# Optimization experiments

Hardware: AMD Instinct MI355X
Metric: run time of the kernel (lower is better)

## Reference

```python
import jax, jax.numpy as jnp
import numpy as np

MEMORY_SIZE = 8192
FEATURE_DIM = 512
NUM_QUERIES = 32768
EPS = 1e-12  # guard for sqrt in cdist


def setup_inputs() -> dict:
    key = jax.random.key(0)
    k1, k2, k3, k4 = jax.random.split(key, 4)
    return {
        "features": jax.random.normal(k1, (MEMORY_SIZE, FEATURE_DIM), dtype=jnp.float32),
        "positions": jax.random.normal(k2, (MEMORY_SIZE, 3), dtype=jnp.float32),
        "query_positions": jax.random.normal(k3, (NUM_QUERIES, 3), dtype=jnp.float32),
        "position_embeddings": jax.random.normal(k4, (MEMORY_SIZE, 3), dtype=jnp.float32),
    }


def _cdist(a, b):
    # Euclidean distance via ||a||^2 + ||b||^2 - 2 a.b; avoids [Q,M,3] intermediate.
    a2 = jnp.sum(a * a, axis=-1, keepdims=True)          # [Q,1]
    b2 = jnp.sum(b * b, axis=-1, keepdims=True).T        # [1,M]
    d2 = a2 + b2 - 2.0 * (a @ b.T)                       # [Q,M]
    return jnp.sqrt(jnp.maximum(d2, EPS))


def reference(features, positions, query_positions, position_embeddings):
    # --- update ---
    positions_norm = positions / jnp.linalg.norm(positions, axis=-1, keepdims=True)
    embeddings_norm = position_embeddings / jnp.linalg.norm(position_embeddings, axis=-1, keepdims=True)
    sim = positions_norm @ embeddings_norm.T             # [M,M]
    attn = jax.nn.softmax(sim, axis=-1)
    memory = attn @ features                              # [M,F]
    new_pos_emb = attn @ positions                        # [M,3]
    # --- query ---
    dist = _cdist(query_positions, new_pos_emb)           # [Q,M]
    qattn = jax.nn.softmax(-dist, axis=-1)
    retrieved = qattn @ memory                            # [Q,F]
    return retrieved
```

## Files before the change

kernel.cpp:

```cpp
#include <hip/hip_runtime.h>
#include <stdint.h>
#include <stddef.h>

#define M_SZ 8192
#define F_DIM 512
#define N_Q 32768

typedef __attribute__((ext_vector_type(4))) float f32x4;
typedef __attribute__((ext_vector_type(8))) __bf16 bf16x8;
typedef __attribute__((ext_vector_type(2))) __bf16 bf16x2;

__device__ __forceinline__ float bits_to_f(unsigned u) {
    union { unsigned u; float f; } v; v.u = u; return v.f;
}
__device__ __forceinline__ unsigned pk_bf16(float a, float b) {
    union { bf16x2 v; unsigned u; } cv;
    cv.v.x = (__bf16)a; cv.v.y = (__bf16)b;
    return cv.u;
}
__device__ __forceinline__ unsigned short f2bf(float x) {
    union { bf16x2 v; unsigned u; } cv;
    cv.v.x = (__bf16)x; cv.v.y = (__bf16)0.0f;
    return (unsigned short)(cv.u & 0xffffu);
}
__device__ __forceinline__ bf16x8 as_bf16x8(uint4 u) {
    union { uint4 a; bf16x8 b; } cv; cv.a = u; return cv.b;
}

__global__ void prep_kernel(const float* __restrict__ pos,
                            const float* __restrict__ emb,
                            float* __restrict__ pn4,
                            float* __restrict__ en4,
                            float* __restrict__ pos4) {
    int i = blockIdx.x * 256 + threadIdx.x;
    if (i >= M_SZ) return;
    float x = pos[i * 3 + 0], y = pos[i * 3 + 1], z = pos[i * 3 + 2];
    float inv = 1.0f / __builtin_amdgcn_sqrtf(x * x + y * y + z * z);
    pn4[i * 4 + 0] = x * inv; pn4[i * 4 + 1] = y * inv;
    pn4[i * 4 + 2] = z * inv; pn4[i * 4 + 3] = 0.0f;
    pos4[i * 4 + 0] = x; pos4[i * 4 + 1] = y;
    pos4[i * 4 + 2] = z; pos4[i * 4 + 3] = 0.0f;
    float ex = emb[i * 3 + 0], ey = emb[i * 3 + 1], ez = emb[i * 3 + 2];
    float einv = 1.0f / __builtin_amdgcn_sqrtf(ex * ex + ey * ey + ez * ez);
    en4[i * 4 + 0] = ex * einv; en4[i * 4 + 1] = ey * einv;
    en4[i * 4 + 2] = ez * einv; en4[i * 4 + 3] = 0.0f;
}

__global__ void transpose_kernel(const float* __restrict__ feat,
                                 unsigned short* __restrict__ featT) {
    __shared__ float tile[64 * 65];
    const int jb = blockIdx.x * 64, fb = blockIdx.y * 64;
    const int t = threadIdx.x;
#pragma unroll
    for (int p = 0; p < 16; ++p) {
        int idx = p * 256 + t;
        int j = idx >> 6, f = idx & 63;
        tile[j * 65 + f] = feat[(size_t)(jb + j) * F_DIM + fb + f];
    }
    __syncthreads();
#pragma unroll
    for (int p = 0; p < 16; ++p) {
        int idx = p * 256 + t;
        int f = idx >> 6, j = idx & 63;
        featT[(size_t)(fb + f) * M_SZ + jb + j] = f2bf(tile[j * 65 + f]);
    }
}

__launch_bounds__(512, 2)
__global__ void build_memory_kernel(const float* __restrict__ pn4,
                                    const float* __restrict__ en4,
                                    const float* __restrict__ pos4,
                                    const unsigned short* __restrict__ featT,
                                    unsigned short* __restrict__ memT,
                                    float* __restrict__ npe4) {
    constexpr int BM = 32, BK = 32, PSTR = BK + 8;
    __shared__ unsigned short pbuf[2][BM * PSTR];
    __shared__ f32x4 red4[512];
    __shared__ float lbuf[BM];

    const int t = threadIdx.x;
    const int lane = t & 63, wv = t >> 6;
    const int col = lane & 15, quad = lane >> 4;
    const int mb = blockIdx.x * BM;
    const int r = t & 31, jq = t >> 5;

    const f32x4 pnr = ((const f32x4*)pn4)[mb + r];
    const f32x4* en = (const f32x4*)en4;
    const f32x4* ps = (const f32x4*)pos4;

    const unsigned short* bp[4];
#pragma unroll
    for (int n = 0; n < 4; ++n)
        bp[n] = featT + (size_t)(wv * 64 + n * 16 + col) * M_SZ + quad * 8;

    f32x4 acc[2][4];
    const f32x4 zero4 = {0.f, 0.f, 0.f, 0.f};
#pragma unroll
    for (int m = 0; m < 2; ++m)
#pragma unroll
        for (int n = 0; n < 4; ++n) acc[m][n] = zero4;
    float nx = 0.f, ny = 0.f, nz = 0.f, lp = 0.f;

    uint4 vbA[4], vbB[4];
#pragma unroll
    for (int n = 0; n < 4; ++n) vbA[n] = *(const uint4*)(bp[n]);

#define B_GEN_P(JB, SIDE)                                                    \
    {                                                                        \
        int j = (JB) + jq * 2;                                               \
        f32x4 e0 = en[j], e1 = en[j + 1];                                    \
        f32x4 p0 = ps[j], p1 = ps[j + 1];                                    \
        float s0 = fmaf(pnr.x, e0.x, fmaf(pnr.y, e0.y, pnr.z * e0.z));       \
        float s1 = fmaf(pnr.x, e1.x, fmaf(pnr.y, e1.y, pnr.z * e1.z));       \
        float w0 = __builtin_amdgcn_exp2f(s0 * 1.44269504f);                 \
        float w1 = __builtin_amdgcn_exp2f(s1 * 1.44269504f);                 \
        unsigned u = pk_bf16(w0, w1);                                        \
        float w0r = bits_to_f(u << 16), w1r = bits_to_f(u & 0xffff0000u);    \
        lp += w0r + w1r;                                                     \
        nx = fmaf(w0r, p0.x, fmaf(w1r, p1.x, nx));                           \
        ny = fmaf(w0r, p0.y, fmaf(w1r, p1.y, ny));                           \
        nz = fmaf(w0r, p0.z, fmaf(w1r, p1.z, nz));                           \
        *(unsigned*)(&pbuf[SIDE][r * PSTR + jq * 2]) = u;                    \
    }

#define B_MFMA(VB, SIDE)                                                     \
    {                                                                        \
        _Pragma("unroll") for (int m = 0; m < 2; ++m) {                      \
            bf16x8 a = *(const bf16x8*)(&pbuf[SIDE][(m * 16 + col) * PSTR + quad * 8]); \
            _Pragma("unroll") for (int n = 0; n < 4; ++n)                    \
                acc[m][n] = __builtin_amdgcn_mfma_f32_16x16x32_bf16(         \
                    a, as_bf16x8(VB[n]), acc[m][n], 0, 0, 0);                \
        }                                                                    \
    }

#define B_BODY(CUR, NXT, SIDE, JNXT)                                         \
    {                                                                        \
        _Pragma("unroll") for (int n = 0; n < 4; ++n) {                      \
            NXT[n] = *(const uint4*)(bp[n] + BK);                            \
            bp[n] += BK;                                                     \
        }                                                                    \
        B_GEN_P(JNXT, SIDE ^ 1)                                              \
        B_MFMA(CUR, SIDE)                                                    \
        __syncthreads();                                                     \
    }

    B_GEN_P(0, 0)
    __syncthreads();

    int jn = BK;
    for (int kt = 0; kt < 254; kt += 2) {
        B_BODY(vbA, vbB, 0, jn) jn += BK;
        B_BODY(vbB, vbA, 1, jn) jn += BK;
    }
    B_BODY(vbA, vbB, 0, jn)
    B_MFMA(vbB, 1)
#undef B_BODY
#undef B_MFMA
#undef B_GEN_P

    f32x4 mine = {nx, ny, nz, lp};
    red4[t] = mine;
    __syncthreads();
    if (t < BM) {
        f32x4 s = red4[t];
#pragma unroll
        for (int g = 1; g < 16; ++g) {
            f32x4 o = red4[t + 32 * g];
            s.x += o.x; s.y += o.y; s.z += o.z; s.w += o.w;
        }
        lbuf[t] = s.w;
        float inv = 1.0f / s.w;
        float X = s.x * inv, Y = s.y * inv, Z = s.z * inv;
        f32x4 o = {X, Y, Z, X * X + Y * Y + Z * Z};
        ((f32x4*)npe4)[mb + t] = o;
    }
    __syncthreads();

#pragma unroll
    for (int m = 0; m < 2; ++m) {
        f32x4 l4 = *(const f32x4*)(lbuf + m * 16 + quad * 4);
        f32x4 inv4 = {1.0f / l4.x, 1.0f / l4.y, 1.0f / l4.z, 1.0f / l4.w};
        int mg = mb + m * 16 + quad * 4;
#pragma unroll
        for (int n = 0; n < 4; ++n) {
            int fg = wv * 64 + n * 16 + col;
            uint2 o;
            o.x = pk_bf16(acc[m][n].x * inv4.x, acc[m][n].y * inv4.y);
            o.y = pk_bf16(acc[m][n].z * inv4.z, acc[m][n].w * inv4.w);
            *(uint2*)(memT + (size_t)fg * M_SZ + mg) = o;
        }
    }
}

__launch_bounds__(512, 2)
__global__ void query_kernel(const float* __restrict__ qpos,
                             const float* __restrict__ npe4,
                             const unsigned short* __restrict__ memT,
                             float* __restrict__ out) {
    constexpr int BM = 128, BK = 32, PSTR = BK + 8;
    __shared__ unsigned short pbuf[2][BM * PSTR];
    __shared__ float redl[512];
    __shared__ float lbuf[BM];

    const int t = threadIdx.x;
    const int lane = t & 63, wv = t >> 6;
    const int col = lane & 15, quad = lane >> 4;
    const int qb = blockIdx.x * BM;
    const int r = t & 127, jq = t >> 7;

    const float qx = qpos[(size_t)(qb + r) * 3 + 0];
    const float qy = qpos[(size_t)(qb + r) * 3 + 1];
    const float qz = qpos[(size_t)(qb + r) * 3 + 2];
    const float q2 = qx * qx + qy * qy + qz * qz;
    const float m2x = -2.0f * qx, m2y = -2.0f * qy, m2z = -2.0f * qz;

    const f32x4* nsrc = (const f32x4*)npe4;

    const unsigned short* bp[4];
#pragma unroll
    for (int n = 0; n < 4; ++n)
        bp[n] = memT + (size_t)(wv * 64 + n * 16 + col) * M_SZ + quad * 8;

    f32x4 acc[8][4];
    const f32x4 zero4 = {0.f, 0.f, 0.f, 0.f};
#pragma unroll
    for (int m = 0; m < 8; ++m)
#pragma unroll
        for (int n = 0; n < 4; ++n) acc[m][n] = zero4;
    float lp = 0.f;

    uint4 vbA[4], vbB[4];
#pragma unroll
    for (int n = 0; n < 4; ++n) vbA[n] = *(const uint4*)(bp[n]);

#define Q_GEN_P(JB, SIDE)                                                    \
    {                                                                        \
        unsigned pk4[4];                                                     \
        _Pragma("unroll") for (int i = 0; i < 8; i += 2) {                   \
            int j = (JB) + jq * 8 + i;                                       \
            f32x4 n0 = nsrc[j], n1 = nsrc[j + 1];                            \
            float s0 = fmaf(m2x, n0.x, fmaf(m2y, n0.y, fmaf(m2z, n0.z, q2 + n0.w))); \
            float s1 = fmaf(m2x, n1.x, fmaf(m2y, n1.y, fmaf(m2z, n1.z, q2 + n1.w))); \
            s0 = fmaxf(s0, 1e-12f); s1 = fmaxf(s1, 1e-12f);                  \
            float w0 = __builtin_amdgcn_exp2f(__builtin_amdgcn_sqrtf(s0) * -1.44269504f); \
            float w1 = __builtin_amdgcn_exp2f(__builtin_amdgcn_sqrtf(s1) * -1.44269504f); \
            unsigned u = pk_bf16(w0, w1);                                    \
            lp += bits_to_f(u << 16) + bits_to_f(u & 0xffff0000u);           \
            pk4[i >> 1] = u;                                                 \
        }                                                                    \
        *(uint4*)(&pbuf[SIDE][r * PSTR + jq * 8]) =                          \
            make_uint4(pk4[0], pk4[1], pk4[2], pk4[3]);                      \
    }

#define Q_MFMA(VB, SIDE)                                                     \
    {                                                                        \
        _Pragma("unroll") for (int m = 0; m < 8; ++m) {                      \
            bf16x8 a = *(const bf16x8*)(&pbuf[SIDE][(m * 16 + col) * PSTR + quad * 8]); \
            _Pragma("unroll") for (int n = 0; n < 4; ++n)                    \
                acc[m][n] = __builtin_amdgcn_mfma_f32_16x16x32_bf16(         \
                    a, as_bf16x8(VB[n]), acc[m][n], 0, 0, 0);                \
        }                                                                    \
    }

#define Q_BODY(CUR, NXT, SIDE, JNXT)                                         \
    {                                                                        \
        _Pragma("unroll") for (int n = 0; n < 4; ++n) {                      \
            NXT[n] = *(const uint4*)(bp[n] + BK);                            \
            bp[n] += BK;                                                     \
        }                                                                    \
        Q_GEN_P(JNXT, SIDE ^ 1)                                              \
        Q_MFMA(CUR, SIDE)                                                    \
        __syncthreads();                                                     \
    }

    Q_GEN_P(0, 0)
    __syncthreads();

    int jn = BK;
    for (int kt = 0; kt < 254; kt += 2) {
        Q_BODY(vbA, vbB, 0, jn) jn += BK;
        Q_BODY(vbB, vbA, 1, jn) jn += BK;
    }
    Q_BODY(vbA, vbB, 0, jn)
    Q_MFMA(vbB, 1)
#undef Q_BODY
#undef Q_MFMA
#undef Q_GEN_P

    redl[t] = lp;
    __syncthreads();
    if (t < BM) lbuf[t] = redl[t] + redl[t + 128] + redl[t + 256] + redl[t + 384];
    __syncthreads();

#pragma unroll
    for (int m = 0; m < 8; ++m) {
        f32x4 l4 = *(const f32x4*)(lbuf + m * 16 + quad * 4);
        f32x4 inv4 = {1.0f / l4.x, 1.0f / l4.y, 1.0f / l4.z, 1.0f / l4.w};
        int qg = qb + m * 16 + quad * 4;
#pragma unroll
        for (int n = 0; n < 4; ++n) {
            int fg = wv * 64 + n * 16 + col;
            out[(size_t)(qg + 0) * F_DIM + fg] = acc[m][n].x * inv4.x;
            out[(size_t)(qg + 1) * F_DIM + fg] = acc[m][n].y * inv4.y;
            out[(size_t)(qg + 2) * F_DIM + fg] = acc[m][n].z * inv4.z;
            out[(size_t)(qg + 3) * F_DIM + fg] = acc[m][n].w * inv4.w;
        }
    }
}

extern "C" void kernel_launch(void* const* d_in, const int* in_sizes, int n_in,
                              void* d_out, int out_size, void* d_ws, size_t ws_size,
                              hipStream_t stream) {
    const float* features  = (const float*)d_in[0];
    const float* positions = (const float*)d_in[1];
    const float* qpos      = (const float*)d_in[2];
    const float* pemb      = (const float*)d_in[3];
    float* out = (float*)d_out;
    char* ws = (char*)d_ws;

    unsigned short* featT = (unsigned short*)(ws);
    unsigned short* memT  = (unsigned short*)(ws + 8388608);
    float* npe4 = (float*)(ws + 16777216);
    float* pn4  = (float*)(ws + 16908288);
    float* en4  = (float*)(ws + 17039360);
    float* pos4 = (float*)(ws + 17170432);

    hipLaunchKernelGGL(prep_kernel, dim3(M_SZ / 256), dim3(256), 0, stream,
                       positions, pemb, pn4, en4, pos4);
    hipLaunchKernelGGL(transpose_kernel, dim3(M_SZ / 64, F_DIM / 64), dim3(256), 0, stream,
                       features, featT);
    hipLaunchKernelGGL(build_memory_kernel, dim3(M_SZ / 32), dim3(512), 0, stream,
                       pn4, en4, pos4, featT, memT, npe4);
    hipLaunchKernelGGL(query_kernel, dim3(N_Q / 128), dim3(512), 0, stream,
                       qpos, npe4, memT, out);
}
```

Measured before the change: 816.3 us.

## Retile build and query kernels to 256-thread blocks with setprio MFMA sections

The build kernel now runs with 256 threads and is split over a second grid dimension covering halves of the feature axis. Only the first half computes the new position embeddings, so the softmax weights are recomputed in both halves. The query kernel shrinks its query tile from 128 to 64 rows and widens each wave's feature tile to 128 columns. Both kernels drop the register double-buffering of B fragments in favour of a single buffer, and wrap their MFMA sections in s_setprio. The aim is more blocks and better occupancy, at the cost of less A-tile reuse, duplicated exp work in the build kernel, and more exposed global load latency.

Result: slower. 1.056 ms (+29.4%).

```diff
diff --git a/kernel.cpp b/kernel.cpp
--- a/kernel.cpp
+++ b/kernel.cpp
@@ -66,7 +66,7 @@
     }
 }
 
-__launch_bounds__(512, 2)
+__launch_bounds__(256, 2)
 __global__ void build_memory_kernel(const float* __restrict__ pn4,
                                     const float* __restrict__ en4,
                                     const float* __restrict__ pos4,
@@ -75,13 +75,14 @@
                                     float* __restrict__ npe4) {
     constexpr int BM = 32, BK = 32, PSTR = BK + 8;
     __shared__ unsigned short pbuf[2][BM * PSTR];
-    __shared__ f32x4 red4[512];
+    __shared__ f32x4 red4[256];
     __shared__ float lbuf[BM];
 
     const int t = threadIdx.x;
     const int lane = t & 63, wv = t >> 6;
     const int col = lane & 15, quad = lane >> 4;
     const int mb = blockIdx.x * BM;
+    const int yh = blockIdx.y;
     const int r = t & 31, jq = t >> 5;
 
     const f32x4 pnr = ((const f32x4*)pn4)[mb + r];
@@ -91,7 +92,7 @@
     const unsigned short* bp[4];
 #pragma unroll
     for (int n = 0; n < 4; ++n)
-        bp[n] = featT + (size_t)(wv * 64 + n * 16 + col) * M_SZ + quad * 8;
+        bp[n] = featT + (size_t)(yh * 256 + wv * 64 + n * 16 + col) * M_SZ + quad * 8;
 
     f32x4 acc[2][4];
     const f32x4 zero4 = {0.f, 0.f, 0.f, 0.f};
@@ -101,62 +102,79 @@
         for (int n = 0; n < 4; ++n) acc[m][n] = zero4;
     float nx = 0.f, ny = 0.f, nz = 0.f, lp = 0.f;
 
-    uint4 vbA[4], vbB[4];
-#pragma unroll
-    for (int n = 0; n < 4; ++n) vbA[n] = *(const uint4*)(bp[n]);
-
-#define B_GEN_P(JB, SIDE)                                                    \
-    {                                                                        \
-        int j = (JB) + jq * 2;                                               \
-        f32x4 e0 = en[j], e1 = en[j + 1];                                    \
-        f32x4 p0 = ps[j], p1 = ps[j + 1];                                    \
-        float s0 = fmaf(pnr.x, e0.x, fmaf(pnr.y, e0.y, pnr.z * e0.z));       \
-        float s1 = fmaf(pnr.x, e1.x, fmaf(pnr.y, e1.y, pnr.z * e1.z));       \
-        float w0 = __builtin_amdgcn_exp2f(s0 * 1.44269504f);                 \
-        float w1 = __builtin_amdgcn_exp2f(s1 * 1.44269504f);                 \
-        unsigned u = pk_bf16(w0, w1);                                        \
-        float w0r = bits_to_f(u << 16), w1r = bits_to_f(u & 0xffff0000u);    \
-        lp += w0r + w1r;                                                     \
-        nx = fmaf(w0r, p0.x, fmaf(w1r, p1.x, nx));                           \
-        ny = fmaf(w0r, p0.y, fmaf(w1r, p1.y, ny));                           \
-        nz = fmaf(w0r, p0.z, fmaf(w1r, p1.z, nz));                           \
-        *(unsigned*)(&pbuf[SIDE][r * PSTR + jq * 2]) = u;                    \
-    }
-
-#define B_MFMA(VB, SIDE)                                                     \
-    {                                                                        \
+    uint4 vb[4];
+
+#define B_COMP(SIDE)                                                         \
+    {                                                                        \
+        float w_[4];                                                         \
+        _Pragma("unroll") for (int i = 0; i < 4; ++i) {                      \
+            float s = fmaf(pnr.x, ee[i].x, fmaf(pnr.y, ee[i].y, pnr.z * ee[i].z)); \
+            w_[i] = __builtin_amdgcn_exp2f(s * 1.44269504f);                 \
+        }                                                                    \
+        unsigned u0 = pk_bf16(w_[0], w_[1]), u1 = pk_bf16(w_[2], w_[3]);     \
+        float wr0 = bits_to_f(u0 << 16), wr1 = bits_to_f(u0 & 0xffff0000u);  \
+        float wr2 = bits_to_f(u1 << 16), wr3 = bits_to_f(u1 & 0xffff0000u);  \
+        lp += (wr0 + wr1) + (wr2 + wr3);                                     \
+        if (yh == 0) {                                                       \
+            nx = fmaf(wr0, pp[0].x, fmaf(wr1, pp[1].x, fmaf(wr2, pp[2].x, fmaf(wr3, pp[3].x, nx)))); \
+            ny = fmaf(wr0, pp[0].y, fmaf(wr1, pp[1].y, fmaf(wr2, pp[2].y, fmaf(wr3, pp[3].y, ny)))); \
+            nz = fmaf(wr0, pp[0].z, fmaf(wr1, pp[1].z, fmaf(wr2, pp[2].z, fmaf(wr3, pp[3].z, nz)))); \
+        }                                                                    \
+        *(uint2*)(&pbuf[SIDE][r * PSTR + jq * 4]) = make_uint2(u0, u1);      \
+    }
+
+#define B_MFMA(SIDE)                                                         \
+    {                                                                        \
+        __builtin_amdgcn_s_setprio(1);                                       \
         _Pragma("unroll") for (int m = 0; m < 2; ++m) {                      \
             bf16x8 a = *(const bf16x8*)(&pbuf[SIDE][(m * 16 + col) * PSTR + quad * 8]); \
             _Pragma("unroll") for (int n = 0; n < 4; ++n)                    \
                 acc[m][n] = __builtin_amdgcn_mfma_f32_16x16x32_bf16(         \
-                    a, as_bf16x8(VB[n]), acc[m][n], 0, 0, 0);                \
-        }                                                                    \
-    }
-
-#define B_BODY(CUR, NXT, SIDE, JNXT)                                         \
-    {                                                                        \
+                    a, as_bf16x8(vb[n]), acc[m][n], 0, 0, 0);                \
+        }                                                                    \
+        __builtin_amdgcn_s_setprio(0);                                       \
+    }
+
+#define B_BODY(SIDE, JNXT)                                                   \
+    {                                                                        \
+        f32x4 ee[4], pp[4];                                                  \
+        _Pragma("unroll") for (int i = 0; i < 4; ++i) {                      \
+            ee[i] = en[(JNXT) + jq * 4 + i];                                 \
+            pp[i] = ps[(JNXT) + jq * 4 + i];                                 \
+        }                                                                    \
         _Pragma("unroll") for (int n = 0; n < 4; ++n) {                      \
-            NXT[n] = *(const uint4*)(bp[n] + BK);                            \
-            bp[n] += BK;                                                     \
-        }                                                                    \
-        B_GEN_P(JNXT, SIDE ^ 1)                                              \
-        B_MFMA(CUR, SIDE)                                                    \
+            vb[n] = *(const uint4*)(bp[n]);  bp[n] += BK;                    \
+        }                                                                    \
+        B_COMP(SIDE ^ 1)                                                     \
+        B_MFMA(SIDE)                                                         \
         __syncthreads();                                                     \
     }
 
-    B_GEN_P(0, 0)
+    {
+        f32x4 ee[4], pp[4];
+#pragma unroll
+        for (int i = 0; i < 4; ++i) {
+            ee[i] = en[jq * 4 + i];
+            pp[i] = ps[jq * 4 + i];
+        }
+        B_COMP(0)
+    }
     __syncthreads();
 
     int jn = BK;
     for (int kt = 0; kt < 254; kt += 2) {
-        B_BODY(vbA, vbB, 0, jn) jn += BK;
-        B_BODY(vbB, vbA, 1, jn) jn += BK;
-    }
-    B_BODY(vbA, vbB, 0, jn)
-    B_MFMA(vbB, 1)
+        B_BODY(0, jn) jn += BK;
+        B_BODY(1, jn) jn += BK;
+    }
+    B_BODY(0, jn)
+    {
+#pragma unroll
+        for (int n = 0; n < 4; ++n) vb[n] = *(const uint4*)(bp[n]);
+        B_MFMA(1)
+    }
 #undef B_BODY
 #undef B_MFMA
-#undef B_GEN_P
+#undef B_COMP
 
     f32x4 mine = {nx, ny, nz, lp};
     red4[t] = mine;
@@ -164,15 +182,17 @@
     if (t < BM) {
         f32x4 s = red4[t];
 #pragma unroll
-        for (int g = 1; g < 16; ++g) {
+        for (int g = 1; g < 8; ++g) {
             f32x4 o = red4[t + 32 * g];
             s.x += o.x; s.y += o.y; s.z += o.z; s.w += o.w;
         }
         lbuf[t] = s.w;
-        float inv = 1.0f / s.w;
-        float X = s.x * inv, Y = s.y * inv, Z = s.z * inv;
-        f32x4 o = {X, Y, Z, X * X + Y * Y + Z * Z};
-        ((f32x4*)npe4)[mb + t] = o;
+        if (yh == 0) {
+            float inv = 1.0f / s.w;
+            float X = s.x * inv, Y = s.y * inv, Z = s.z * inv;
+            f32x4 o = {X, Y, Z, X * X + Y * Y + Z * Z};
+            ((f32x4*)npe4)[mb + t] = o;
+        }
     }
     __syncthreads();
 
@@ -183,7 +203,7 @@
         int mg = mb + m * 16 + quad * 4;
 #pragma unroll
         for (int n = 0; n < 4; ++n) {
-            int fg = wv * 64 + n * 16 + col;
+            int fg = yh * 256 + wv * 64 + n * 16 + col;
             uint2 o;
             o.x = pk_bf16(acc[m][n].x * inv4.x, acc[m][n].y * inv4.y);
             o.y = pk_bf16(acc[m][n].z * inv4.z, acc[m][n].w * inv4.w);
@@ -192,21 +212,21 @@
     }
 }
 
-__launch_bounds__(512, 2)
+__launch_bounds__(256, 2)
 __global__ void query_kernel(const float* __restrict__ qpos,
                              const float* __restrict__ npe4,
                              const unsigned short* __restrict__ memT,
                              float* __restrict__ out) {
-    constexpr int BM = 128, BK = 32, PSTR = BK + 8;
+    constexpr int BM = 64, BK = 32, PSTR = BK + 8;
     __shared__ unsigned short pbuf[2][BM * PSTR];
-    __shared__ float redl[512];
+    __shared__ float redl[256];
     __shared__ float lbuf[BM];
 
     const int t = threadIdx.x;
     const int lane = t & 63, wv = t >> 6;
     const int col = lane & 15, quad = lane >> 4;
     const int qb = blockIdx.x * BM;
-    const int r = t & 127, jq = t >> 7;
+    const int r = t & 63, jq = t >> 6;
 
     const float qx = qpos[(size_t)(qb + r) * 3 + 0];
     const float qy = qpos[(size_t)(qb + r) * 3 + 1];
@@ -216,31 +236,27 @@
 
     const f32x4* nsrc = (const f32x4*)npe4;
 
-    const unsigned short* bp[4];
-#pragma unroll
-    for (int n = 0; n < 4; ++n)
-        bp[n] = memT + (size_t)(wv * 64 + n * 16 + col) * M_SZ + quad * 8;
-
-    f32x4 acc[8][4];
+    const unsigned short* bp[8];
+#pragma unroll
+    for (int n = 0; n < 8; ++n)
+        bp[n] = memT + (size_t)(wv * 128 + n * 16 + col) * M_SZ + quad * 8;
+
+    f32x4 acc[4][8];
     const f32x4 zero4 = {0.f, 0.f, 0.f, 0.f};
 #pragma unroll
-    for (int m = 0; m < 8; ++m)
-#pragma unroll
-        for (int n = 0; n < 4; ++n) acc[m][n] = zero4;
+    for (int m = 0; m < 4; ++m)
+#pragma unroll
+        for (int n = 0; n < 8; ++n) acc[m][n] = zero4;
     float lp = 0.f;
 
-    uint4 vbA[4], vbB[4];
-#pragma unroll
-    for (int n = 0; n < 4; ++n) vbA[n] = *(const uint4*)(bp[n]);
-
-#define Q_GEN_P(JB, SIDE)                                                    \
+    uint4 vb[8];
+
+#define Q_COMP(SIDE)                                                         \
     {                                                                        \
         unsigned pk4[4];                                                     \
         _Pragma("unroll") for (int i = 0; i < 8; i += 2) {                   \
-            int j = (JB) + jq * 8 + i;                                       \
-            f32x4 n0 = nsrc[j], n1 = nsrc[j + 1];                            \
-            float s0 = fmaf(m2x, n0.x, fmaf(m2y, n0.y, fmaf(m2z, n0.z, q2 + n0.w))); \
-            float s1 = fmaf(m2x, n1.x, fmaf(m2y, n1.y, fmaf(m2z, n1.z, q2 + n1.w))); \
+            float s0 = fmaf(m2x, nn[i].x, fmaf(m2y, nn[i].y, fmaf(m2z, nn[i].z, q2 + nn[i].w))); \
+            float s1 = fmaf(m2x, nn[i + 1].x, fmaf(m2y, nn[i + 1].y, fmaf(m2z, nn[i + 1].z, q2 + nn[i + 1].w))); \
             s0 = fmaxf(s0, 1e-12f); s1 = fmaxf(s1, 1e-12f);                  \
             float w0 = __builtin_amdgcn_exp2f(__builtin_amdgcn_sqrtf(s0) * -1.44269504f); \
             float w1 = __builtin_amdgcn_exp2f(__builtin_amdgcn_sqrtf(s1) * -1.44269504f); \
@@ -252,54 +268,67 @@
             make_uint4(pk4[0], pk4[1], pk4[2], pk4[3]);                      \
     }
 
-#define Q_MFMA(VB, SIDE)                                                     \
-    {                                                                        \
-        _Pragma("unroll") for (int m = 0; m < 8; ++m) {                      \
+#define Q_MFMA(SIDE)                                                         \
+    {                                                                        \
+        __builtin_amdgcn_s_setprio(1);                                       \
+        _Pragma("unroll") for (int m = 0; m < 4; ++m) {                      \
             bf16x8 a = *(const bf16x8*)(&pbuf[SIDE][(m * 16 + col) * PSTR + quad * 8]); \
-            _Pragma("unroll") for (int n = 0; n < 4; ++n)                    \
+            _Pragma("unroll") for (int n = 0; n < 8; ++n)                    \
                 acc[m][n] = __builtin_amdgcn_mfma_f32_16x16x32_bf16(         \
-                    a, as_bf16x8(VB[n]), acc[m][n], 0, 0, 0);                \
-        }                                                                    \
-    }
-
-#define Q_BODY(CUR, NXT, SIDE, JNXT)                                         \
-    {                                                                        \
-        _Pragma("unroll") for (int n = 0; n < 4; ++n) {                      \
-            NXT[n] = *(const uint4*)(bp[n] + BK);                            \
-            bp[n] += BK;                                                     \
-        }                                                                    \
-        Q_GEN_P(JNXT, SIDE ^ 1)                                              \
-        Q_MFMA(CUR, SIDE)                                                    \
+                    a, as_bf16x8(vb[n]), acc[m][n], 0, 0, 0);                \
+        }                                                                    \
+        __builtin_amdgcn_s_setprio(0);                                       \
+    }
+
+#define Q_BODY(SIDE, JNXT)                                                   \
+    {                                                                        \
+        f32x4 nn[8];                                                         \
+        _Pragma("unroll") for (int i = 0; i < 8; ++i)                        \
+            nn[i] = nsrc[(JNXT) + jq * 8 + i];                               \
+        _Pragma("unroll") for (int n = 0; n < 8; ++n) {                      \
+            vb[n] = *(const uint4*)(bp[n]);  bp[n] += BK;                    \
+        }                                                                    \
+        Q_COMP(SIDE ^ 1)                                                     \
+        Q_MFMA(SIDE)                                                         \
         __syncthreads();                                                     \
     }
 
-    Q_GEN_P(0, 0)
+    {
+        f32x4 nn[8];
+#pragma unroll
+        for (int i = 0; i < 8; ++i) nn[i] = nsrc[jq * 8 + i];
+        Q_COMP(0)
+    }
     __syncthreads();
 
     int jn = BK;
     for (int kt = 0; kt < 254; kt += 2) {
-        Q_BODY(vbA, vbB, 0, jn) jn += BK;
-        Q_BODY(vbB, vbA, 1, jn) jn += BK;
-    }
-    Q_BODY(vbA, vbB, 0, jn)
-    Q_MFMA(vbB, 1)
+        Q_BODY(0, jn) jn += BK;
+        Q_BODY(1, jn) jn += BK;
+    }
+    Q_BODY(0, jn)
+    {
+#pragma unroll
+        for (int n = 0; n < 8; ++n) vb[n] = *(const uint4*)(bp[n]);
+        Q_MFMA(1)
+    }
 #undef Q_BODY
 #undef Q_MFMA
-#undef Q_GEN_P
+#undef Q_COMP
 
     redl[t] = lp;
     __syncthreads();
-    if (t < BM) lbuf[t] = redl[t] + redl[t + 128] + redl[t + 256] + redl[t + 384];
-    __syncthreads();
-
-#pragma unroll
-    for (int m = 0; m < 8; ++m) {
+    if (t < BM) lbuf[t] = redl[t] + redl[t + 64] + redl[t + 128] + redl[t + 192];
+    __syncthreads();
+
+#pragma unroll
+    for (int m = 0; m < 4; ++m) {
         f32x4 l4 = *(const f32x4*)(lbuf + m * 16 + quad * 4);
         f32x4 inv4 = {1.0f / l4.x, 1.0f / l4.y, 1.0f / l4.z, 1.0f / l4.w};
         int qg = qb + m * 16 + quad * 4;
 #pragma unroll
-        for (int n = 0; n < 4; ++n) {
-            int fg = wv * 64 + n * 16 + col;
+        for (int n = 0; n < 8; ++n) {
+            int fg = wv * 128 + n * 16 + col;
             out[(size_t)(qg + 0) * F_DIM + fg] = acc[m][n].x * inv4.x;
             out[(size_t)(qg + 1) * F_DIM + fg] = acc[m][n].y * inv4.y;
             out[(size_t)(qg + 2) * F_DIM + fg] = acc[m][n].z * inv4.z;
@@ -329,8 +358,8 @@
                        positions, pemb, pn4, en4, pos4);
     hipLaunchKernelGGL(transpose_kernel, dim3(M_SZ / 64, F_DIM / 64), dim3(256), 0, stream,
                        features, featT);
-    hipLaunchKernelGGL(build_memory_kernel, dim3(M_SZ / 32), dim3(512), 0, stream,
+    hipLaunchKernelGGL(build_memory_kernel, dim3(M_SZ / 32, 2), dim3(256), 0, stream,
                        pn4, en4, pos4, featT, memT, npe4);
-    hipLaunchKernelGGL(query_kernel, dim3(N_Q / 128), dim3(512), 0, stream,
+    hipLaunchKernelGGL(query_kernel, dim3(N_Q / 64), dim3(256), 0, stream,
                        qpos, npe4, memT, out);
 }
```

## Retile memory-build GEMM to 128 rows by 128 features and double K-step

Applied to the files above, without the earlier changes.

The build kernel moves from 32-row blocks covering all 512 features to 128-row blocks that each cover a quarter of the feature dimension, with four blocks per row group. Each block now computes four times as many softmax weights per feature-column load and issues eight MFMAs per B fragment instead of two. Both the build and query kernels double the K-step from 32 to 64, which halves the number of barriers and loop iterations. The trade-off is that the exp and softmax weight work in the build kernel is now repeated four times across the feature splits, and more registers are used per wave.

After: 887.4 us. +8.7%, slower.

```diff
diff --git a/kernel.cpp b/kernel.cpp
--- a/kernel.cpp
+++ b/kernel.cpp
@@ -73,7 +73,7 @@
                                     const unsigned short* __restrict__ featT,
                                     unsigned short* __restrict__ memT,
                                     float* __restrict__ npe4) {
-    constexpr int BM = 32, BK = 32, PSTR = BK + 8;
+    constexpr int BM = 128, BK = 64, PSTR = BK + 8;
     __shared__ unsigned short pbuf[2][BM * PSTR];
     __shared__ f32x4 red4[512];
     __shared__ float lbuf[BM];
@@ -81,82 +81,92 @@
     const int t = threadIdx.x;
     const int lane = t & 63, wv = t >> 6;
     const int col = lane & 15, quad = lane >> 4;
-    const int mb = blockIdx.x * BM;
-    const int r = t & 31, jq = t >> 5;
+    const int bid = blockIdx.x;
+    const int fb = bid & 3;
+    const int mb = (bid >> 2) * BM;
+    const int r = t & 127, jq = t >> 7;
 
     const f32x4 pnr = ((const f32x4*)pn4)[mb + r];
     const f32x4* en = (const f32x4*)en4;
     const f32x4* ps = (const f32x4*)pos4;
 
-    const unsigned short* bp[4];
-#pragma unroll
-    for (int n = 0; n < 4; ++n)
-        bp[n] = featT + (size_t)(wv * 64 + n * 16 + col) * M_SZ + quad * 8;
-
-    f32x4 acc[2][4];
+    const unsigned short* bp =
+        featT + (size_t)(fb * 128 + wv * 16 + col) * M_SZ + quad * 8;
+
+    f32x4 acc[8];
     const f32x4 zero4 = {0.f, 0.f, 0.f, 0.f};
 #pragma unroll
-    for (int m = 0; m < 2; ++m)
-#pragma unroll
-        for (int n = 0; n < 4; ++n) acc[m][n] = zero4;
+    for (int m = 0; m < 8; ++m) acc[m] = zero4;
     float nx = 0.f, ny = 0.f, nz = 0.f, lp = 0.f;
 
-    uint4 vbA[4], vbB[4];
-#pragma unroll
-    for (int n = 0; n < 4; ++n) vbA[n] = *(const uint4*)(bp[n]);
-
-#define B_GEN_P(JB, SIDE)                                                    \
-    {                                                                        \
-        int j = (JB) + jq * 2;                                               \
-        f32x4 e0 = en[j], e1 = en[j + 1];                                    \
-        f32x4 p0 = ps[j], p1 = ps[j + 1];                                    \
-        float s0 = fmaf(pnr.x, e0.x, fmaf(pnr.y, e0.y, pnr.z * e0.z));       \
-        float s1 = fmaf(pnr.x, e1.x, fmaf(pnr.y, e1.y, pnr.z * e1.z));       \
-        float w0 = __builtin_amdgcn_exp2f(s0 * 1.44269504f);                 \
-        float w1 = __builtin_amdgcn_exp2f(s1 * 1.44269504f);                 \
-        unsigned u = pk_bf16(w0, w1);                                        \
-        float w0r = bits_to_f(u << 16), w1r = bits_to_f(u & 0xffff0000u);    \
-        lp += w0r + w1r;                                                     \
-        nx = fmaf(w0r, p0.x, fmaf(w1r, p1.x, nx));                           \
-        ny = fmaf(w0r, p0.y, fmaf(w1r, p1.y, ny));                           \
-        nz = fmaf(w0r, p0.z, fmaf(w1r, p1.z, nz));                           \
-        *(unsigned*)(&pbuf[SIDE][r * PSTR + jq * 2]) = u;                    \
-    }
-
-#define B_MFMA(VB, SIDE)                                                     \
-    {                                                                        \
-        _Pragma("unroll") for (int m = 0; m < 2; ++m) {                      \
-            bf16x8 a = *(const bf16x8*)(&pbuf[SIDE][(m * 16 + col) * PSTR + quad * 8]); \
-            _Pragma("unroll") for (int n = 0; n < 4; ++n)                    \
-                acc[m][n] = __builtin_amdgcn_mfma_f32_16x16x32_bf16(         \
-                    a, as_bf16x8(VB[n]), acc[m][n], 0, 0, 0);                \
-        }                                                                    \
-    }
-
-#define B_BODY(CUR, NXT, SIDE, JNXT)                                         \
-    {                                                                        \
-        _Pragma("unroll") for (int n = 0; n < 4; ++n) {                      \
-            NXT[n] = *(const uint4*)(bp[n] + BK);                            \
-            bp[n] += BK;                                                     \
-        }                                                                    \
-        B_GEN_P(JNXT, SIDE ^ 1)                                              \
-        B_MFMA(CUR, SIDE)                                                    \
+    uint4 h0A, h0B, h1v;
+    h0A = *(const uint4*)(bp);
+
+#define B_COMP(JB, SIDE)                                                     \
+    {                                                                        \
+        _Pragma("unroll") for (int hh = 0; hh < 2; ++hh) {                   \
+            unsigned us[4];                                                  \
+            _Pragma("unroll") for (int i = 0; i < 8; i += 2) {               \
+                int j = (JB) + jq * 16 + hh * 8 + i;                         \
+                f32x4 e0 = en[j], e1 = en[j + 1];                            \
+                f32x4 p0 = ps[j], p1 = ps[j + 1];                            \
+                float s0 = fmaf(pnr.x, e0.x, fmaf(pnr.y, e0.y, pnr.z * e0.z)); \
+                float s1 = fmaf(pnr.x, e1.x, fmaf(pnr.y, e1.y, pnr.z * e1.z)); \
+                float w0 = __builtin_amdgcn_exp2f(s0 * 1.44269504f);         \
+                float w1 = __builtin_amdgcn_exp2f(s1 * 1.44269504f);         \
+                unsigned u = pk_bf16(w0, w1);                                \
+                float w0r = bits_to_f(u << 16), w1r = bits_to_f(u & 0xffff0000u); \
+                lp += w0r + w1r;                                             \
+                nx = fmaf(w0r, p0.x, fmaf(w1r, p1.x, nx));                   \
+                ny = fmaf(w0r, p0.y, fmaf(w1r, p1.y, ny));                   \
+                nz = fmaf(w0r, p0.z, fmaf(w1r, p1.z, nz));                   \
+                us[i >> 1] = u;                                              \
+            }                                                                \
+            *(uint4*)(&pbuf[(SIDE)][r * PSTR + jq * 16 + hh * 8]) =          \
+                make_uint4(us[0], us[1], us[2], us[3]);                      \
+        }                                                                    \
+    }
+
+#define B_MFMA(SIDE, VB0, VB1)                                               \
+    {                                                                        \
+        _Pragma("unroll") for (int m = 0; m < 8; ++m) {                      \
+            bf16x8 a = *(const bf16x8*)(&pbuf[(SIDE)][(m * 16 + col) * PSTR + quad * 8]); \
+            acc[m] = __builtin_amdgcn_mfma_f32_16x16x32_bf16(                \
+                a, as_bf16x8(VB0), acc[m], 0, 0, 0);                         \
+        }                                                                    \
+        _Pragma("unroll") for (int m = 0; m < 8; ++m) {                      \
+            bf16x8 a = *(const bf16x8*)(&pbuf[(SIDE)][(m * 16 + col) * PSTR + 32 + quad * 8]); \
+            acc[m] = __builtin_amdgcn_mfma_f32_16x16x32_bf16(                \
+                a, as_bf16x8(VB1), acc[m], 0, 0, 0);                         \
+        }                                                                    \
+    }
+
+#define B_BODY(CURH0, NXTH0, SIDE, JNXT)                                     \
+    {                                                                        \
+        h1v = *(const uint4*)(bp + 32);                                      \
+        NXTH0 = *(const uint4*)(bp + 64);                                    \
+        bp += 64;                                                            \
+        B_COMP(JNXT, (SIDE) ^ 1)                                             \
+        B_MFMA(SIDE, CURH0, h1v)                                             \
         __syncthreads();                                                     \
     }
 
-    B_GEN_P(0, 0)
+    B_COMP(0, 0)
     __syncthreads();
 
     int jn = BK;
-    for (int kt = 0; kt < 254; kt += 2) {
-        B_BODY(vbA, vbB, 0, jn) jn += BK;
-        B_BODY(vbB, vbA, 1, jn) jn += BK;
-    }
-    B_BODY(vbA, vbB, 0, jn)
-    B_MFMA(vbB, 1)
+    for (int kt = 0; kt < 126; kt += 2) {
+        B_BODY(h0A, h0B, 0, jn) jn += BK;
+        B_BODY(h0B, h0A, 1, jn) jn += BK;
+    }
+    B_BODY(h0A, h0B, 0, jn)
+    {
+        h1v = *(const uint4*)(bp + 32);
+        B_MFMA(1, h0B, h1v)
+    }
 #undef B_BODY
 #undef B_MFMA
-#undef B_GEN_P
+#undef B_COMP
 
     f32x4 mine = {nx, ny, nz, lp};
     red4[t] = mine;
@@ -164,29 +174,30 @@
     if (t < BM) {
         f32x4 s = red4[t];
 #pragma unroll
-        for (int g = 1; g < 16; ++g) {
-            f32x4 o = red4[t + 32 * g];
+        for (int g = 1; g < 4; ++g) {
+            f32x4 o = red4[t + 128 * g];
             s.x += o.x; s.y += o.y; s.z += o.z; s.w += o.w;
         }
         lbuf[t] = s.w;
-        float inv = 1.0f / s.w;
-        float X = s.x * inv, Y = s.y * inv, Z = s.z * inv;
-        f32x4 o = {X, Y, Z, X * X + Y * Y + Z * Z};
-        ((f32x4*)npe4)[mb + t] = o;
-    }
-    __syncthreads();
-
-#pragma unroll
-    for (int m = 0; m < 2; ++m) {
-        f32x4 l4 = *(const f32x4*)(lbuf + m * 16 + quad * 4);
-        f32x4 inv4 = {1.0f / l4.x, 1.0f / l4.y, 1.0f / l4.z, 1.0f / l4.w};
-        int mg = mb + m * 16 + quad * 4;
-#pragma unroll
-        for (int n = 0; n < 4; ++n) {
-            int fg = wv * 64 + n * 16 + col;
+        if (fb == 0) {
+            float inv = 1.0f / s.w;
+            float X = s.x * inv, Y = s.y * inv, Z = s.z * inv;
+            f32x4 o = {X, Y, Z, X * X + Y * Y + Z * Z};
+            ((f32x4*)npe4)[mb + t] = o;
+        }
+    }
+    __syncthreads();
+
+    {
+        int fg = fb * 128 + wv * 16 + col;
+#pragma unroll
+        for (int m = 0; m < 8; ++m) {
+            f32x4 l4 = *(const f32x4*)(lbuf + m * 16 + quad * 4);
+            f32x4 inv4 = {1.0f / l4.x, 1.0f / l4.y, 1.0f / l4.z, 1.0f / l4.w};
+            int mg = mb + m * 16 + quad * 4;
             uint2 o;
-            o.x = pk_bf16(acc[m][n].x * inv4.x, acc[m][n].y * inv4.y);
-            o.y = pk_bf16(acc[m][n].z * inv4.z, acc[m][n].w * inv4.w);
+            o.x = pk_bf16(acc[m].x * inv4.x, acc[m].y * inv4.y);
+            o.y = pk_bf16(acc[m].z * inv4.z, acc[m].w * inv4.w);
             *(uint2*)(memT + (size_t)fg * M_SZ + mg) = o;
         }
     }
@@ -197,7 +208,7 @@
                              const float* __restrict__ npe4,
                              const unsigned short* __restrict__ memT,
                              float* __restrict__ out) {
-    constexpr int BM = 128, BK = 32, PSTR = BK + 8;
+    constexpr int BM = 128, BK = 64, PSTR = BK + 8;
     __shared__ unsigned short pbuf[2][BM * PSTR];
     __shared__ float redl[512];
     __shared__ float lbuf[BM];
@@ -229,63 +240,77 @@
         for (int n = 0; n < 4; ++n) acc[m][n] = zero4;
     float lp = 0.f;
 
-    uint4 vbA[4], vbB[4];
-#pragma unroll
-    for (int n = 0; n < 4; ++n) vbA[n] = *(const uint4*)(bp[n]);
-
-#define Q_GEN_P(JB, SIDE)                                                    \
-    {                                                                        \
-        unsigned pk4[4];                                                     \
-        _Pragma("unroll") for (int i = 0; i < 8; i += 2) {                   \
-            int j = (JB) + jq * 8 + i;                                       \
-            f32x4 n0 = nsrc[j], n1 = nsrc[j + 1];                            \
-            float s0 = fmaf(m2x, n0.x, fmaf(m2y, n0.y, fmaf(m2z, n0.z, q2 + n0.w))); \
-            float s1 = fmaf(m2x, n1.x, fmaf(m2y, n1.y, fmaf(m2z, n1.z, q2 + n1.w))); \
-            s0 = fmaxf(s0, 1e-12f); s1 = fmaxf(s1, 1e-12f);                  \
-            float w0 = __builtin_amdgcn_exp2f(__builtin_amdgcn_sqrtf(s0) * -1.44269504f); \
-            float w1 = __builtin_amdgcn_exp2f(__builtin_amdgcn_sqrtf(s1) * -1.44269504f); \
-            unsigned u = pk_bf16(w0, w1);                                    \
-            lp += bits_to_f(u << 16) + bits_to_f(u & 0xffff0000u);           \
-            pk4[i >> 1] = u;                                                 \
-        }                                                                    \
-        *(uint4*)(&pbuf[SIDE][r * PSTR + jq * 8]) =                          \
-            make_uint4(pk4[0], pk4[1], pk4[2], pk4[3]);                      \
-    }
-
-#define Q_MFMA(VB, SIDE)                                                     \
+    uint4 h0A[4], h0B[4], h1[4];
+#pragma unroll
+    for (int n = 0; n < 4; ++n) h0A[n] = *(const uint4*)(bp[n]);
+
+#define Q_COMP(JB, SIDE)                                                     \
+    {                                                                        \
+        _Pragma("unroll") for (int hh = 0; hh < 2; ++hh) {                   \
+            unsigned us[4];                                                  \
+            _Pragma("unroll") for (int i = 0; i < 8; i += 2) {               \
+                int j = (JB) + jq * 16 + hh * 8 + i;                         \
+                f32x4 n0 = nsrc[j], n1 = nsrc[j + 1];                        \
+                float s0 = fmaf(m2x, n0.x, fmaf(m2y, n0.y, fmaf(m2z, n0.z, q2 + n0.w))); \
+                float s1 = fmaf(m2x, n1.x, fmaf(m2y, n1.y, fmaf(m2z, n1.z, q2 + n1.w))); \
+                s0 = fmaxf(s0, 1e-12f); s1 = fmaxf(s1, 1e-12f);              \
+                float w0 = __builtin_amdgcn_exp2f(__builtin_amdgcn_sqrtf(s0) * -1.44269504f); \
+                float w1 = __builtin_amdgcn_exp2f(__builtin_amdgcn_sqrtf(s1) * -1.44269504f); \
+                unsigned u = pk_bf16(w0, w1);                                \
+                lp += bits_to_f(u << 16) + bits_to_f(u & 0xffff0000u);       \
+                us[i >> 1] = u;                                              \
+            }                                                                \
+            *(uint4*)(&pbuf[(SIDE)][r * PSTR + jq * 16 + hh * 8]) =          \
+                make_uint4(us[0], us[1], us[2], us[3]);                      \
+        }                                                                    \
+    }
+
+#define Q_MFMA(SIDE, VB0, VB1)                                               \
     {                                                                        \
         _Pragma("unroll") for (int m = 0; m < 8; ++m) {                      \
-            bf16x8 a = *(const bf16x8*)(&pbuf[SIDE][(m * 16 + col) * PSTR + quad * 8]); \
+            bf16x8 a = *(const bf16x8*)(&pbuf[(SIDE)][(m * 16 + col) * PSTR + quad * 8]); \
             _Pragma("unroll") for (int n = 0; n < 4; ++n)                    \
                 acc[m][n] = __builtin_amdgcn_mfma_f32_16x16x32_bf16(         \
-                    a, as_bf16x8(VB[n]), acc[m][n], 0, 0, 0);                \
-        }                                                                    \
-    }
-
-#define Q_BODY(CUR, NXT, SIDE, JNXT)                                         \
-    {                                                                        \
+                    a, as_bf16x8(VB0[n]), acc[m][n], 0, 0, 0);               \
+        }                                                                    \
+        _Pragma("unroll") for (int m = 0; m < 8; ++m) {                      \
+            bf16x8 a = *(const bf16x8*)(&pbuf[(SIDE)][(m * 16 + col) * PSTR + 32 + quad * 8]); \
+            _Pragma("unroll") for (int n = 0; n < 4; ++n)                    \
+                acc[m][n] = __builtin_amdgcn_mfma_f32_16x16x32_bf16(         \
+                    a, as_bf16x8(VB1[n]), acc[m][n], 0, 0, 0);               \
+        }                                                                    \
+    }
+
+#define Q_BODY(CURH0, NXTH0, SIDE, JNXT)                                     \
+    {                                                                        \
+        _Pragma("unroll") for (int n = 0; n < 4; ++n)                        \
+            h1[n] = *(const uint4*)(bp[n] + 32);                             \
         _Pragma("unroll") for (int n = 0; n < 4; ++n) {                      \
-            NXT[n] = *(const uint4*)(bp[n] + BK);                            \
-            bp[n] += BK;                                                     \
-        }                                                                    \
-        Q_GEN_P(JNXT, SIDE ^ 1)                                              \
-        Q_MFMA(CUR, SIDE)                                                    \
+            NXTH0[n] = *(const uint4*)(bp[n] + 64);                          \
+            bp[n] += 64;                                                     \
+        }                                                                    \
+        Q_COMP(JNXT, (SIDE) ^ 1)                                             \
+        Q_MFMA(SIDE, CURH0, h1)                                              \
         __syncthreads();                                                     \
     }
 
-    Q_GEN_P(0, 0)
+    Q_COMP(0, 0)
     __syncthreads();
 
     int jn = BK;
-    for (int kt = 0; kt < 254; kt += 2) {
-        Q_BODY(vbA, vbB, 0, jn) jn += BK;
-        Q_BODY(vbB, vbA, 1, jn) jn += BK;
-    }
-    Q_BODY(vbA, vbB, 0, jn)
-    Q_MFMA(vbB, 1)
+    for (int kt = 0; kt < 126; kt += 2) {
+        Q_BODY(h0A, h0B, 0, jn) jn += BK;
+        Q_BODY(h0B, h0A, 1, jn) jn += BK;
+    }
+    Q_BODY(h0A, h0B, 0, jn)
+    {
+#pragma unroll
+        for (int n = 0; n < 4; ++n) h1[n] = *(const uint4*)(bp[n] + 32);
+        Q_MFMA(1, h0B, h1)
+    }
 #undef Q_BODY
 #undef Q_MFMA
-#undef Q_GEN_P
+#undef Q_COMP
 
     redl[t] = lp;
     __syncthreads();
@@ -329,7 +354,7 @@
                        positions, pemb, pn4, en4, pos4);
     hipLaunchKernelGGL(transpose_kernel, dim3(M_SZ / 64, F_DIM / 64), dim3(256), 0, stream,
                        features, featT);
-    hipLaunchKernelGGL(build_memory_kernel, dim3(M_SZ / 32), dim3(512), 0, stream,
+    hipLaunchKernelGGL(build_memory_kernel, dim3((M_SZ / 128) * 4), dim3(512), 0, stream,
                        pn4, en4, pos4, featT, memT, npe4);
     hipLaunchKernelGGL(query_kernel, dim3(N_Q / 128), dim3(512), 0, stream,
                        qpos, npe4, memT, out);
```
